# Kernel tuning notes

Hardware: AMD Instinct MI355X
Metric: run time of the kernel (lower is better)

## Reference

```python
import jax, jax.numpy as jnp
import numpy as np

N_LIG, N_TGT, E = 100000, 20000, 1000000
H = 128

def setup_inputs() -> dict:
    key = jax.random.key(0)
    ks = jax.random.split(key, 20)
    def lin(k, fan_in, fan_out):
        k1, k2 = jax.random.split(k)
        lim = 1.0 / np.sqrt(fan_in)
        W = jax.random.uniform(k1, (fan_in, fan_out), jnp.float32, -lim, lim)
        b = jax.random.uniform(k2, (fan_out,), jnp.float32, -lim, lim)
        return W, b
    W_lig, b_lig = lin(ks[0], 4, H)
    W_tgt, b_tgt = lin(ks[1], 1280, H)
    W1f, b1f = lin(ks[2], H, H)   # conv1 ligand->target
    W1r, b1r = lin(ks[3], H, H)   # conv1 target->ligand
    W2f, b2f = lin(ks[4], H, H)   # conv2 ligand->target
    W2r, b2r = lin(ks[5], H, H)   # conv2 target->ligand
    Wp1, bp1 = lin(ks[6], 2 * H, H)  # lin1
    Wp2, bp2 = lin(ks[7], H, 1)      # lin2
    return {
        'x_ligand': jax.random.normal(ks[8], (N_LIG, 4), jnp.float32),
        'x_target': jax.random.normal(ks[9], (N_TGT, 1280), jnp.float32),
        'edge_src': jax.random.randint(ks[10], (E,), 0, N_LIG, jnp.int32),
        'edge_dst': jax.random.randint(ks[11], (E,), 0, N_TGT, jnp.int32),
        'W_lig': W_lig, 'b_lig': b_lig, 'W_tgt': W_tgt, 'b_tgt': b_tgt,
        'W1f': W1f, 'b1f': b1f, 'W1r': W1r, 'b1r': b1r,
        'W2f': W2f, 'b2f': b2f, 'W2r': W2r, 'b2r': b2r,
        'Wp1': Wp1, 'bp1': bp1, 'Wp2': Wp2, 'bp2': bp2,
    }

def _mean_agg(feat, idx, num_segments):
    # scatter-mean: sum / count, 0 for isolated nodes (matches PyG 'mean')
    s = jax.ops.segment_sum(feat, idx, num_segments=num_segments)
    cnt = jax.ops.segment_sum(jnp.ones((idx.shape[0],), feat.dtype), idx,
                              num_segments=num_segments)
    return s / jnp.maximum(cnt, 1.0)[:, None]

def reference(x_ligand, x_target, edge_src, edge_dst,
              W_lig, b_lig, W_tgt, b_tgt,
              W1f, b1f, W1r, b1r, W2f, b2f, W2r, b2r,
              Wp1, bp1, Wp2, bp2):
    h_lig = x_ligand @ W_lig + b_lig   # [N_lig, H]
    h_tgt = x_target @ W_tgt + b_tgt   # [N_tgt, H]

    def conv(h_lig, h_tgt, Wf, bf, Wr, br):
        # ligand -> target (edges as given), target -> ligand (flipped edges)
        agg_t = _mean_agg(h_lig[edge_src], edge_dst, h_tgt.shape[0])
        agg_l = _mean_agg(h_tgt[edge_dst], edge_src, h_lig.shape[0])
        new_tgt = jax.nn.relu(agg_t @ Wf + bf)
        new_lig = jax.nn.relu(agg_l @ Wr + br)
        return new_lig, new_tgt

    h_lig, h_tgt = conv(h_lig, h_tgt, W1f, b1f, W1r, b1r)
    h_lig, h_tgt = conv(h_lig, h_tgt, W2f, b2f, W2r, b2r)

    # per-edge prediction (vectorized gather + tiny MLP), original loops edges
    combined = jnp.concatenate([h_lig[edge_src], h_tgt[edge_dst]], axis=-1)  # [E, 2H]
    pred = jax.nn.relu(combined @ Wp1 + bp1) @ Wp2 + bp2                     # [E, 1]
    return pred
```

## Files before the change

### kernel.cpp

```cpp
#include <hip/hip_runtime.h>
#include <hip/hip_bf16.h>

#define N_LIG 100000
#define N_TGT 20000
#define NEDGE 1000000
#define H 128
#define NXCD 8
#define RL 12500
#define RT 2500
#define CAP 131072
#define NSLICE 32

typedef __attribute__((ext_vector_type(8))) short short8v;
typedef __attribute__((ext_vector_type(4))) float f32x4;

__device__ __forceinline__ unsigned short f2bs(float f) {
    unsigned int u = __float_as_uint(f);
    u += 0x7fff + ((u >> 16) & 1);
    return (unsigned short)(u >> 16);
}
__device__ __forceinline__ float bs2f(unsigned int s) {
    return __uint_as_float(s << 16);
}

__global__ void transpose_w(const float* __restrict__ W, unsigned short* __restrict__ Wt, int K) {
    int idx = blockIdx.x * blockDim.x + threadIdx.x;
    if (idx >= K * 128) return;
    int k = idx >> 7, c = idx & 127;
    Wt[(size_t)c * K + k] = f2bs(W[idx]);
}

struct P6 { const float* w[6]; unsigned short* o[6]; };
__global__ void transpose6(P6 p) {
    int idx = blockIdx.x * blockDim.x + threadIdx.x;
    int which = idx >> 14;
    int rem = idx & 16383;
    int k = rem >> 7, c = rem & 127;
    p.o[which][(size_t)c * 128 + k] = f2bs(p.w[which][rem]);
}

__global__ void lin4_bf16(const float* __restrict__ X, const float* __restrict__ W,
                          const float* __restrict__ b, unsigned short* __restrict__ Y, int N) {
    int idx = blockIdx.x * blockDim.x + threadIdx.x;
    if (idx >= N * 16) return;
    int r = idx >> 4;
    int c = (idx & 15) * 8;
    float x0 = X[r * 4 + 0], x1 = X[r * 4 + 1], x2 = X[r * 4 + 2], x3 = X[r * 4 + 3];
    unsigned int o[4];
#pragma unroll
    for (int p = 0; p < 4; ++p) {
        float v0 = b[c + 2 * p] + x0 * W[c + 2 * p] + x1 * W[H + c + 2 * p] +
                   x2 * W[2 * H + c + 2 * p] + x3 * W[3 * H + c + 2 * p];
        float v1 = b[c + 2 * p + 1] + x0 * W[c + 2 * p + 1] + x1 * W[H + c + 2 * p + 1] +
                   x2 * W[2 * H + c + 2 * p + 1] + x3 * W[3 * H + c + 2 * p + 1];
        o[p] = (unsigned int)f2bs(v0) | ((unsigned int)f2bs(v1) << 16);
    }
    uint4 u = make_uint4(o[0], o[1], o[2], o[3]);
    *(uint4*)&Y[(size_t)r * H + c] = u;
}

__launch_bounds__(256)
__global__ void gemm_bf16(const unsigned short* __restrict__ X,
                          const float* __restrict__ Xf32,
                          const unsigned short* __restrict__ Wt,
                          const float* __restrict__ bias,
                          unsigned short* __restrict__ Y,
                          float* __restrict__ Yf,
                          int N, int K, int do_relu) {
    __shared__ unsigned short Ws[128 * 128];
    const int t = threadIdx.x;
    const int wv = t >> 6;
    const int lane = t & 63;
    const int lr = lane & 15;
    const int kb = lane >> 4;
    const int row0 = blockIdx.x * 64 + wv * 16;

    f32x4 acc[8];
#pragma unroll
    for (int i = 0; i < 8; ++i) acc[i] = (f32x4){0.f, 0.f, 0.f, 0.f};

    int arow = row0 + lr;
    if (arow >= N) arow = N - 1;
    const unsigned short* xrow = X ? X + (size_t)arow * K : nullptr;
    const float* xrowf = Xf32 ? Xf32 + (size_t)arow * K : nullptr;

    const int nch = K >> 7;
    for (int kc = 0; kc < nch; ++kc) {
        if (kc) __syncthreads();
#pragma unroll
        for (int i = 0; i < 8; ++i) {
            int li = t + i * 256;
            int r = li >> 4;
            int cb = (li & 15) << 4;
            int4 v = *(const int4*)(Wt + (size_t)r * K + (kc << 7) + (cb >> 1));
            *(int4*)((char*)Ws + r * 256 + (cb ^ ((r & 7) << 4))) = v;
        }
        short8v a[4];
        if (xrow) {
#pragma unroll
            for (int ks = 0; ks < 4; ++ks)
                a[ks] = *(const short8v*)(xrow + (kc << 7) + ks * 32 + kb * 8);
        } else {
#pragma unroll
            for (int ks = 0; ks < 4; ++ks) {
                const float* p = xrowf + (kc << 7) + ks * 32 + kb * 8;
                float4 f0 = *(const float4*)p;
                float4 f1 = *(const float4*)(p + 4);
                short8v av;
                av[0] = (short)f2bs(f0.x); av[1] = (short)f2bs(f0.y);
                av[2] = (short)f2bs(f0.z); av[3] = (short)f2bs(f0.w);
                av[4] = (short)f2bs(f1.x); av[5] = (short)f2bs(f1.y);
                av[6] = (short)f2bs(f1.z); av[7] = (short)f2bs(f1.w);
                a[ks] = av;
            }
        }
        __syncthreads();
#pragma unroll
        for (int ks = 0; ks < 4; ++ks) {
            int ofs = ks * 64 + kb * 16;
#pragma unroll
            for (int ct = 0; ct < 8; ++ct) {
                int c = ct * 16 + lr;
                short8v b = *(const short8v*)((const char*)Ws + c * 256 + (ofs ^ ((c & 7) << 4)));
                acc[ct] = __builtin_amdgcn_mfma_f32_16x16x32_bf16(a[ks], b, acc[ct], 0, 0, 0);
            }
        }
    }
#pragma unroll
    for (int ct = 0; ct < 8; ++ct) {
        int col = ct * 16 + lr;
        float bv = bias ? bias[col] : 0.f;
#pragma unroll
        for (int r = 0; r < 4; ++r) {
            int grow = row0 + kb * 4 + r;
            if (grow < N) {
                float v = acc[ct][r] + bv;
                if (do_relu) v = fmaxf(v, 0.f);
                if (Yf) Yf[(size_t)grow * H + col] = v;
                else    Y[(size_t)grow * H + col] = f2bs(v);
            }
        }
    }
}

__global__ void zero_gcur(int* __restrict__ g) {
    if (threadIdx.x < 16) g[threadIdx.x] = 0;
}

__launch_bounds__(256)
__global__ void bin_edges(const int* __restrict__ es, const int* __restrict__ ed,
                          unsigned long long* __restrict__ bkt_l, unsigned int* __restrict__ bkt_t,
                          int* __restrict__ gcur, int E) {
    __shared__ int h[16];
    __shared__ int base_s[16];
    int t = threadIdx.x;
    int lane = t & 63;
    if (t < 16) h[t] = 0;
    __syncthreads();
    int chunk = (E + gridDim.x - 1) / gridDim.x;
    int beg = blockIdx.x * chunk;
    int end = min(beg + chunk, E);
    for (int e0 = beg; e0 < end; e0 += 256) {
        int e = e0 + t;
        int bl = -1, bt = -1;
        if (e < end) { bl = es[e] / RL; bt = ed[e] / RT; }
#pragma unroll
        for (int b = 0; b < 8; ++b) {
            unsigned long long m = __ballot(bl == b);
            if (lane == 0 && m) atomicAdd(&h[b], __popcll(m));
            m = __ballot(bt == b);
            if (lane == 0 && m) atomicAdd(&h[8 + b], __popcll(m));
        }
    }
    __syncthreads();
    if (t < 16) {
        base_s[t] = atomicAdd(&gcur[t], h[t]);
        h[t] = 0;
    }
    __syncthreads();
    for (int e0 = beg; e0 < end; e0 += 256) {
        int e = e0 + t;
        int s = 0, d = 0, bl = -1, bt = -1;
        if (e < end) { s = es[e]; d = ed[e]; bl = s / RL; bt = d / RT; }
        unsigned int low = ((unsigned int)d << 17) | (unsigned int)s;
#pragma unroll
        for (int b = 0; b < 8; ++b) {
            unsigned long long m = __ballot(bl == b);
            if (m) {
                int leader = __ffsll((unsigned long long)m) - 1;
                int rank = __popcll(m & ((1ULL << lane) - 1ULL));
                int wbase = 0;
                if (lane == leader) wbase = atomicAdd(&h[b], __popcll(m));
                wbase = __shfl(wbase, leader);
                if (bl == b) {
                    int i = min(base_s[b] + wbase + rank, CAP - 1);
                    bkt_l[(size_t)b * CAP + i] = ((unsigned long long)(unsigned int)e << 32) | low;
                }
            }
            m = __ballot(bt == b);
            if (m) {
                int leader = __ffsll((unsigned long long)m) - 1;
                int rank = __popcll(m & ((1ULL << lane) - 1ULL));
                int wbase = 0;
                if (lane == leader) wbase = atomicAdd(&h[8 + b], __popcll(m));
                wbase = __shfl(wbase, leader);
                if (bt == b) {
                    int i = min(base_s[8 + b] + wbase + rank, CAP - 1);
                    bkt_t[(size_t)b * CAP + i] = low;
                }
            }
        }
    }
}

__launch_bounds__(256)
__global__ void count_slices(const unsigned long long* __restrict__ bkt_l,
                             const unsigned int* __restrict__ bkt_t,
                             const int* __restrict__ gcur,
                             int* __restrict__ cnts_l, int* __restrict__ cnts_t) {
    __shared__ int h[RL];
    int bi = blockIdx.x;
    int t = threadIdx.x;
    if (bi < 256) {
        int p = bi & 7, slice = bi >> 3;
        for (int j = t; j < RL; j += 256) h[j] = 0;
        __syncthreads();
        int n = min(gcur[p], CAP);
        int ss = (n + NSLICE - 1) / NSLICE;
        int beg = slice * ss, end = min(beg + ss, n);
        const unsigned long long* b = bkt_l + (size_t)p * CAP;
        for (int i = beg + t; i < end; i += 256)
            atomicAdd(&h[((unsigned int)b[i] & 0x1FFFF) - p * RL], 1);
        __syncthreads();
        int* dst = cnts_l + (size_t)slice * N_LIG + p * RL;
        for (int j = t; j < RL; j += 256) dst[j] = h[j];
    } else {
        int k = bi - 256;
        int p = k & 7, slice = k >> 3;
        for (int j = t; j < RT; j += 256) h[j] = 0;
        __syncthreads();
        int n = min(gcur[8 + p], CAP);
        int ss = (n + NSLICE - 1) / NSLICE;
        int beg = slice * ss, end = min(beg + ss, n);
        const unsigned int* b = bkt_t + (size_t)p * CAP;
        for (int i = beg + t; i < end; i += 256)
            atomicAdd(&h[(int)(b[i] >> 17) - p * RT], 1);
        __syncthreads();
        int* dst = cnts_t + (size_t)slice * N_TGT + p * RT;
        for (int j = t; j < RT; j += 256) dst[j] = h[j];
    }
}

__global__ void scan_block2(int* __restrict__ cnts_l, int* __restrict__ out_l,
                            int* __restrict__ bs_l, int nL, int nbL,
                            int* __restrict__ cnts_t, int* __restrict__ out_t,
                            int* __restrict__ bs_t, int nT) {
    __shared__ int ts[256];
    int* cnts; int* out; int* bsum; int n; int bi; size_t N;
    if ((int)blockIdx.x < nbL) { cnts = cnts_l; out = out_l; bsum = bs_l; n = nL; bi = blockIdx.x; N = N_LIG; }
    else { cnts = cnts_t; out = out_t; bsum = bs_t; n = nT; bi = blockIdx.x - nbL; N = N_TGT; }
    int t = threadIdx.x;
    int base = bi * 1024 + t * 4;
    int v[4] = {0, 0, 0, 0};
    for (int sl = 0; sl < NSLICE; ++sl) {
        size_t o = (size_t)sl * N + base;
#pragma unroll
        for (int i = 0; i < 4; i++) {
            if (base + i < n) {
                int c = cnts[o + i];
                cnts[o + i] = v[i];
                v[i] += c;
            }
        }
    }
    int s = v[0] + v[1] + v[2] + v[3];
    ts[t] = s;
    __syncthreads();
    for (int ofs = 1; ofs < 256; ofs <<= 1) {
        int x = (t >= ofs) ? ts[t - ofs] : 0;
        __syncthreads();
        ts[t] += x;
        __syncthreads();
    }
    int run = (t == 0) ? 0 : ts[t - 1];
    if (t == 255) bsum[bi] = ts[255];
#pragma unroll
    for (int i = 0; i < 4; i++) {
        if (base + i < n) out[base + i] = run;
        run += v[i];
    }
}

__global__ void scan_top2(int* __restrict__ bs_l, int nbL, int* __restrict__ bs_t, int nbT) {
    __shared__ int ts[256];
    int* bsum = (blockIdx.x == 0) ? bs_l : bs_t;
    int nb = (blockIdx.x == 0) ? nbL : nbT;
    int t = threadIdx.x;
    ts[t] = (t < nb) ? bsum[t] : 0;
    __syncthreads();
    for (int ofs = 1; ofs < 256; ofs <<= 1) {
        int x = (t >= ofs) ? ts[t - ofs] : 0;
        __syncthreads();
        ts[t] += x;
        __syncthreads();
    }
    int excl = (t == 0) ? 0 : ts[t - 1];
    if (t < nb) bsum[t] = excl;
}

__global__ void add_off2(int* __restrict__ rp_l, const int* __restrict__ bs_l,
                         int* __restrict__ rp_t, const int* __restrict__ bs_t) {
    int i = blockIdx.x * blockDim.x + threadIdx.x;
    if (i < N_LIG) {
        rp_l[i] += bs_l[i >> 10];
        if (i == 0) rp_l[N_LIG] = NEDGE;
    } else if (i < N_LIG + N_TGT) {
        int j = i - N_LIG;
        rp_t[j] += bs_t[j >> 10];
        if (j == 0) rp_t[N_TGT] = NEDGE;
    }
}

__launch_bounds__(256)
__global__ void fill_slices(const unsigned long long* __restrict__ bkt_l,
                            const unsigned int* __restrict__ bkt_t,
                            const int* __restrict__ gcur,
                            const int* __restrict__ rowptr_l, const int* __restrict__ rowptr_t,
                            const int* __restrict__ cnts_l, const int* __restrict__ cnts_t,
                            int2* __restrict__ elist_l, int* __restrict__ nbr_t) {
    __shared__ int cur[RL];
    int bi = blockIdx.x;
    int t = threadIdx.x;
    if (bi < 256) {
        int p = bi & 7, slice = bi >> 3;
        const int* rp = rowptr_l + p * RL;
        const int* pf = cnts_l + (size_t)slice * N_LIG + p * RL;
        for (int j = t; j < RL; j += 256) cur[j] = rp[j] + pf[j];
        __syncthreads();
        int n = min(gcur[p], CAP);
        int ss = (n + NSLICE - 1) / NSLICE;
        int beg = slice * ss, end = min(beg + ss, n);
        const unsigned long long* b = bkt_l + (size_t)p * CAP;
        for (int i = beg + t; i < end; i += 256) {
            unsigned long long v = b[i];
            unsigned int low = (unsigned int)v;
            int pos = atomicAdd(&cur[(low & 0x1FFFF) - p * RL], 1);
            elist_l[pos] = make_int2((low >> 17) & 0x7FFF, (int)(v >> 32));
        }
    } else {
        int k = bi - 256;
        int p = k & 7, slice = k >> 3;
        const int* rp = rowptr_t + p * RT;
        const int* pf = cnts_t + (size_t)slice * N_TGT + p * RT;
        for (int j = t; j < RT; j += 256) cur[j] = rp[j] + pf[j];
        __syncthreads();
        int n = min(gcur[8 + p], CAP);
        int ss = (n + NSLICE - 1) / NSLICE;
        int beg = slice * ss, end = min(beg + ss, n);
        const unsigned int* b = bkt_t + (size_t)p * CAP;
        for (int i = beg + t; i < end; i += 256) {
            unsigned int v = b[i];
            int pos = atomicAdd(&cur[(v >> 17) - p * RT], 1);
            nbr_t[pos] = v & 0x1FFFF;
        }
    }
}

__launch_bounds__(256)
__global__ void gather_mean_bf16(const unsigned short* __restrict__ feat,
                                 const int* __restrict__ rowptr, const int* __restrict__ nbr,
                                 int stride, const float* __restrict__ bias,
                                 unsigned short* __restrict__ out, int N) {
    int wid = (blockIdx.x * blockDim.x + threadIdx.x) >> 6;
    if (wid >= N) return;
    int lane = threadIdx.x & 63;
    int beg = rowptr[wid], end = rowptr[wid + 1];
    const unsigned int* f = (const unsigned int*)feat;
    float ax = 0.f, ay = 0.f;
    int j = beg;
    for (; j + 8 <= end; j += 8) {
        unsigned int v[8];
#pragma unroll
        for (int q = 0; q < 8; ++q) v[q] = f[(size_t)nbr[(j + q) * stride] * 64 + lane];
#pragma unroll
        for (int q = 0; q < 8; ++q) { ax += bs2f(v[q] & 0xffff); ay += bs2f(v[q] >> 16); }
    }
    for (; j + 2 <= end; j += 2) {
        unsigned int v0 = f[(size_t)nbr[(j + 0) * stride] * 64 + lane];
        unsigned int v1 = f[(size_t)nbr[(j + 1) * stride] * 64 + lane];
        ax += bs2f(v0 & 0xffff) + bs2f(v1 & 0xffff);
        ay += bs2f(v0 >> 16) + bs2f(v1 >> 16);
    }
    for (; j < end; ++j) {
        unsigned int v = f[(size_t)nbr[j * stride] * 64 + lane];
        ax += bs2f(v & 0xffff);
        ay += bs2f(v >> 16);
    }
    float inv = 1.f / (float)max(end - beg, 1);
    float mx = ax * inv, my = ay * inv;
    if (bias) {
        mx = fmaxf(mx + bias[2 * lane], 0.f);
        my = fmaxf(my + bias[2 * lane + 1], 0.f);
    }
    unsigned int o = (unsigned int)f2bs(mx) | ((unsigned int)f2bs(my) << 16);
    ((unsigned int*)out)[(size_t)wid * 64 + lane] = o;
}

__launch_bounds__(256)
__global__ void edge_mlp_csr(const unsigned short* __restrict__ A16, const unsigned short* __restrict__ B16,
                             const int* __restrict__ rowptr, const int2* __restrict__ elist,
                             const float* __restrict__ Wp2, const float* __restrict__ bp2,
                             float* __restrict__ out, int N) {
    int w = (blockIdx.x * blockDim.x + threadIdx.x) >> 6;
    if (w >= N) return;
    int lane = threadIdx.x & 63;
    int g = lane >> 4, l16 = lane & 15;
    int beg = rowptr[w], end = rowptr[w + 1];
    if (beg == end) return;
    uint4 ua = *(const uint4*)&A16[(size_t)w * H + l16 * 8];
    float a[8] = {bs2f(ua.x & 0xffff), bs2f(ua.x >> 16), bs2f(ua.y & 0xffff), bs2f(ua.y >> 16),
                  bs2f(ua.z & 0xffff), bs2f(ua.z >> 16), bs2f(ua.w & 0xffff), bs2f(ua.w >> 16)};
    float4 w0 = *(const float4*)&Wp2[l16 * 8];
    float4 w1 = *(const float4*)&Wp2[l16 * 8 + 4];
    float wv[8] = {w0.x, w0.y, w0.z, w0.w, w1.x, w1.y, w1.z, w1.w};
    float bp = bp2[0];
    for (int p = beg + g; p < end; p += 4) {
        int2 de = elist[p];
        uint4 ub = *(const uint4*)&B16[(size_t)de.x * H + l16 * 8];
        float bb[8] = {bs2f(ub.x & 0xffff), bs2f(ub.x >> 16), bs2f(ub.y & 0xffff), bs2f(ub.y >> 16),
                       bs2f(ub.z & 0xffff), bs2f(ub.z >> 16), bs2f(ub.w & 0xffff), bs2f(ub.w >> 16)};
        float acc = 0.f;
#pragma unroll
        for (int q = 0; q < 8; ++q) acc += fmaxf(a[q] + bb[q], 0.f) * wv[q];
        acc += __shfl_xor(acc, 8);
        acc += __shfl_xor(acc, 4);
        acc += __shfl_xor(acc, 2);
        acc += __shfl_xor(acc, 1);
        if (l16 == 0) out[de.y] = acc + bp;
    }
}

extern "C" void kernel_launch(void* const* d_in, const int* in_sizes, int n_in,
                              void* d_out, int out_size, void* d_ws, size_t ws_size,
                              hipStream_t stream) {
    const float* x_lig = (const float*)d_in[0];
    const float* x_tgt = (const float*)d_in[1];
    const int* es = (const int*)d_in[2];
    const int* ed = (const int*)d_in[3];
    const float* W_lig = (const float*)d_in[4];
    const float* b_lig = (const float*)d_in[5];
    const float* W_tgt = (const float*)d_in[6];
    const float* b_tgt = (const float*)d_in[7];
    const float* W1f = (const float*)d_in[8];
    const float* b1f = (const float*)d_in[9];
    const float* W1r = (const float*)d_in[10];
    const float* b1r = (const float*)d_in[11];
    const float* W2f = (const float*)d_in[12];
    const float* b2f = (const float*)d_in[13];
    const float* W2r = (const float*)d_in[14];
    const float* b2r = (const float*)d_in[15];
    const float* Wp1 = (const float*)d_in[16];
    const float* bp1 = (const float*)d_in[17];
    const float* Wp2 = (const float*)d_in[18];
    const float* bp2 = (const float*)d_in[19];
    float* out = (float*)d_out;

    char* base = (char*)d_ws;
    size_t off = 0;
    auto alloc = [&](size_t bytes) { char* p = base + off; off = (off + bytes + 255) & ~(size_t)255; return p; };
    unsigned short* L0 = (unsigned short*)alloc((size_t)N_LIG * H * 2);
    unsigned short* L1 = (unsigned short*)alloc((size_t)N_LIG * H * 2);
    unsigned short* T0 = (unsigned short*)alloc((size_t)N_TGT * H * 2);
    unsigned short* T1 = (unsigned short*)alloc((size_t)N_TGT * H * 2);
    unsigned short* G  = (unsigned short*)alloc((size_t)N_TGT * H * 2);
    unsigned short* Wt_tgt = (unsigned short*)alloc((size_t)128 * 1280 * 2);
    unsigned short* Wt1f = (unsigned short*)alloc(128 * 128 * 2);
    unsigned short* Wt1r = (unsigned short*)alloc(128 * 128 * 2);
    unsigned short* Wt2f = (unsigned short*)alloc(128 * 128 * 2);
    unsigned short* Wt2r = (unsigned short*)alloc(128 * 128 * 2);
    unsigned short* WtA = (unsigned short*)alloc(128 * 128 * 2);
    unsigned short* WtB = (unsigned short*)alloc(128 * 128 * 2);
    int* cnts_l = (int*)alloc((size_t)NSLICE * N_LIG * 4);
    int* cnts_t = (int*)alloc((size_t)NSLICE * N_TGT * 4);
    int* rowptr_l = (int*)alloc((N_LIG + 4) * 4);
    int* rowptr_t = (int*)alloc((N_TGT + 4) * 4);
    int* bsum_l = (int*)alloc(256 * 4);
    int* bsum_t = (int*)alloc(256 * 4);
    int* gcur = (int*)alloc(16 * 4);
    int2* elist_l = (int2*)alloc((size_t)NEDGE * 8);
    int* nbr_t = (int*)alloc((size_t)NEDGE * 4);
    unsigned long long* bkt_l = (unsigned long long*)alloc((size_t)NXCD * CAP * 8);
    unsigned int* bkt_t = (unsigned int*)alloc((size_t)NXCD * CAP * 4);

    const int ligBlocks = (N_LIG + 63) / 64;
    const int tgtBlocks = (N_TGT + 63) / 64;
    const int nbL = (N_LIG + 1023) / 1024;
    const int nbT = (N_TGT + 1023) / 1024;

    transpose_w<<<(1280 * 128 + 255) / 256, 256, 0, stream>>>(W_tgt, Wt_tgt, 1280);
    P6 p6;
    p6.w[0] = W1f; p6.o[0] = Wt1f;
    p6.w[1] = W1r; p6.o[1] = Wt1r;
    p6.w[2] = W2f; p6.o[2] = Wt2f;
    p6.w[3] = W2r; p6.o[3] = Wt2r;
    p6.w[4] = Wp1;           p6.o[4] = WtA;
    p6.w[5] = Wp1 + 128 * H; p6.o[5] = WtB;
    transpose6<<<6 * 64, 256, 0, stream>>>(p6);

    lin4_bf16<<<(N_LIG * 16 + 255) / 256, 256, 0, stream>>>(x_lig, W_lig, b_lig, L0, N_LIG);
    gemm_bf16<<<tgtBlocks, 256, 0, stream>>>(nullptr, x_tgt, Wt_tgt, b_tgt, T0, nullptr, N_TGT, 1280, 0);

    zero_gcur<<<1, 64, 0, stream>>>(gcur);
    bin_edges<<<512, 256, 0, stream>>>(es, ed, bkt_l, bkt_t, gcur, NEDGE);
    count_slices<<<512, 256, 0, stream>>>(bkt_l, bkt_t, gcur, cnts_l, cnts_t);
    scan_block2<<<nbL + nbT, 256, 0, stream>>>(cnts_l, rowptr_l, bsum_l, N_LIG, nbL,
                                               cnts_t, rowptr_t, bsum_t, N_TGT);
    scan_top2<<<2, 256, 0, stream>>>(bsum_l, nbL, bsum_t, nbT);
    add_off2<<<(N_LIG + N_TGT + 255) / 256, 256, 0, stream>>>(rowptr_l, bsum_l, rowptr_t, bsum_t);
    fill_slices<<<512, 256, 0, stream>>>(bkt_l, bkt_t, gcur, rowptr_l, rowptr_t,
                                         cnts_l, cnts_t, elist_l, nbr_t);

    const unsigned short* Wtf[2] = {Wt1f, Wt2f};
    const float* bfp[2] = {b1f, b2f};
    const unsigned short* Wtr[2] = {Wt1r, Wt2r};
    const float* brp[2] = {b1r, b2r};
    for (int layer = 0; layer < 2; ++layer) {
        gemm_bf16<<<tgtBlocks, 256, 0, stream>>>(T0, nullptr, Wtr[layer], nullptr, G, nullptr, N_TGT, 128, 0);
        gather_mean_bf16<<<(N_TGT * 64 + 255) / 256, 256, 0, stream>>>(L0, rowptr_t, nbr_t, 1, nullptr, T1, N_TGT);
        gather_mean_bf16<<<(N_LIG * 64 + 255) / 256, 256, 0, stream>>>(G, rowptr_l, (const int*)elist_l, 2, brp[layer], L0, N_LIG);
        gemm_bf16<<<tgtBlocks, 256, 0, stream>>>(T1, nullptr, Wtf[layer], bfp[layer], T0, nullptr, N_TGT, 128, 1);
    }

    gemm_bf16<<<ligBlocks, 256, 0, stream>>>(L0, nullptr, WtA, nullptr, L1, nullptr, N_LIG, 128, 0);
    gemm_bf16<<<tgtBlocks, 256, 0, stream>>>(T0, nullptr, WtB, bp1, T1, nullptr, N_TGT, 128, 0);

    edge_mlp_csr<<<(N_LIG * 64 + 255) / 256, 256, 0, stream>>>(
        L1, T1, rowptr_l, elist_l, Wp2, bp2, out, N_LIG);
}
```

Baseline: 459.7 us.

## Merge both mean-gathers into one launch with 16-byte loads across four edges

The two per-layer gather_mean kernels become a single gather2 launch. Its first N_TGT waves handle targets and the rest handle ligands. The ligand output now ping-pongs between two buffers, so the kernel no longer reads and writes L0 at the same time. Each wave now splits into four 16-lane groups that gather different edges with 128-bit loads per lane, then reduces the groups with cross-lane shuffles. This cuts the number of memory instructions and exposes more loads in flight. Non-temporal load and store hints are added to index reads and to the edge-MLP input and output, and the shuffle reduction adds some extra ALU work.

```diff
diff --git a/kernel.cpp b/kernel.cpp
--- a/kernel.cpp
+++ b/kernel.cpp
@@ -13,6 +13,7 @@
 
 typedef __attribute__((ext_vector_type(8))) short short8v;
 typedef __attribute__((ext_vector_type(4))) float f32x4;
+typedef __attribute__((ext_vector_type(4))) unsigned int uint4v;
 
 __device__ __forceinline__ unsigned short f2bs(float f) {
     unsigned int u = __float_as_uint(f);
@@ -367,43 +368,68 @@
 }
 
 __launch_bounds__(256)
-__global__ void gather_mean_bf16(const unsigned short* __restrict__ feat,
-                                 const int* __restrict__ rowptr, const int* __restrict__ nbr,
-                                 int stride, const float* __restrict__ bias,
-                                 unsigned short* __restrict__ out, int N) {
-    int wid = (blockIdx.x * blockDim.x + threadIdx.x) >> 6;
-    if (wid >= N) return;
+__global__ void gather2(const unsigned short* __restrict__ L_in, const int* __restrict__ rp_t,
+                        const int* __restrict__ nbr_t, unsigned short* __restrict__ T_out,
+                        const unsigned short* __restrict__ G, const int* __restrict__ rp_l,
+                        const int* __restrict__ elist2, const float* __restrict__ bias_r,
+                        unsigned short* __restrict__ L_out) {
+    int gwid = (blockIdx.x * blockDim.x + threadIdx.x) >> 6;
     int lane = threadIdx.x & 63;
-    int beg = rowptr[wid], end = rowptr[wid + 1];
-    const unsigned int* f = (const unsigned int*)feat;
-    float ax = 0.f, ay = 0.f;
-    int j = beg;
-    for (; j + 8 <= end; j += 8) {
-        unsigned int v[8];
-#pragma unroll
-        for (int q = 0; q < 8; ++q) v[q] = f[(size_t)nbr[(j + q) * stride] * 64 + lane];
-#pragma unroll
-        for (int q = 0; q < 8; ++q) { ax += bs2f(v[q] & 0xffff); ay += bs2f(v[q] >> 16); }
-    }
-    for (; j + 2 <= end; j += 2) {
-        unsigned int v0 = f[(size_t)nbr[(j + 0) * stride] * 64 + lane];
-        unsigned int v1 = f[(size_t)nbr[(j + 1) * stride] * 64 + lane];
-        ax += bs2f(v0 & 0xffff) + bs2f(v1 & 0xffff);
-        ay += bs2f(v0 >> 16) + bs2f(v1 >> 16);
-    }
-    for (; j < end; ++j) {
-        unsigned int v = f[(size_t)nbr[j * stride] * 64 + lane];
-        ax += bs2f(v & 0xffff);
-        ay += bs2f(v >> 16);
-    }
-    float inv = 1.f / (float)max(end - beg, 1);
-    float mx = ax * inv, my = ay * inv;
-    if (bias) {
-        mx = fmaxf(mx + bias[2 * lane], 0.f);
-        my = fmaxf(my + bias[2 * lane + 1], 0.f);
-    }
-    unsigned int o = (unsigned int)f2bs(mx) | ((unsigned int)f2bs(my) << 16);
-    ((unsigned int*)out)[(size_t)wid * 64 + lane] = o;
+    int g = lane >> 4, l16 = lane & 15;
+    const unsigned short* feat;
+    const int* rp;
+    const int* nbr;
+    int stride, wid;
+    const float* bias;
+    unsigned short* outp;
+    if (gwid < N_TGT) {
+        feat = L_in; rp = rp_t; nbr = nbr_t; stride = 1; bias = nullptr; outp = T_out; wid = gwid;
+    } else if (gwid < N_TGT + N_LIG) {
+        feat = G; rp = rp_l; nbr = elist2; stride = 2; bias = bias_r; outp = L_out; wid = gwid - N_TGT;
+    } else return;
+    int beg = rp[wid], end = rp[wid + 1];
+    const uint4v* f4 = (const uint4v*)feat;
+    float acc[8] = {0.f, 0.f, 0.f, 0.f, 0.f, 0.f, 0.f, 0.f};
+    int j = beg + g;
+    for (; j + 4 < end; j += 8) {
+        int n0 = __builtin_nontemporal_load(&nbr[j * stride]);
+        int n1 = __builtin_nontemporal_load(&nbr[(j + 4) * stride]);
+        uint4v v0 = f4[(size_t)n0 * 16 + l16];
+        uint4v v1 = f4[(size_t)n1 * 16 + l16];
+#pragma unroll
+        for (int q = 0; q < 4; ++q) {
+            acc[2 * q] += bs2f(v0[q] & 0xffff) + bs2f(v1[q] & 0xffff);
+            acc[2 * q + 1] += bs2f(v0[q] >> 16) + bs2f(v1[q] >> 16);
+        }
+    }
+    for (; j < end; j += 4) {
+        int n0 = __builtin_nontemporal_load(&nbr[j * stride]);
+        uint4v v0 = f4[(size_t)n0 * 16 + l16];
+#pragma unroll
+        for (int q = 0; q < 4; ++q) {
+            acc[2 * q] += bs2f(v0[q] & 0xffff);
+            acc[2 * q + 1] += bs2f(v0[q] >> 16);
+        }
+    }
+#pragma unroll
+    for (int q = 0; q < 8; ++q) {
+        acc[q] += __shfl_xor(acc[q], 16);
+        acc[q] += __shfl_xor(acc[q], 32);
+    }
+    if (g == 0) {
+        float inv = 1.f / (float)max(end - beg, 1);
+        uint4v o;
+#pragma unroll
+        for (int q = 0; q < 4; ++q) {
+            float m0 = acc[2 * q] * inv, m1 = acc[2 * q + 1] * inv;
+            if (bias) {
+                m0 = fmaxf(m0 + bias[l16 * 8 + 2 * q], 0.f);
+                m1 = fmaxf(m1 + bias[l16 * 8 + 2 * q + 1], 0.f);
+            }
+            o[q] = (unsigned int)f2bs(m0) | ((unsigned int)f2bs(m1) << 16);
+        }
+        ((uint4v*)outp)[(size_t)wid * 16 + l16] = o;
+    }
 }
 
 __launch_bounds__(256)
@@ -417,26 +443,29 @@
     int g = lane >> 4, l16 = lane & 15;
     int beg = rowptr[w], end = rowptr[w + 1];
     if (beg == end) return;
-    uint4 ua = *(const uint4*)&A16[(size_t)w * H + l16 * 8];
-    float a[8] = {bs2f(ua.x & 0xffff), bs2f(ua.x >> 16), bs2f(ua.y & 0xffff), bs2f(ua.y >> 16),
-                  bs2f(ua.z & 0xffff), bs2f(ua.z >> 16), bs2f(ua.w & 0xffff), bs2f(ua.w >> 16)};
+    uint4v ua = __builtin_nontemporal_load((const uint4v*)&A16[(size_t)w * H + l16 * 8]);
+    float a[8] = {bs2f(ua[0] & 0xffff), bs2f(ua[0] >> 16), bs2f(ua[1] & 0xffff), bs2f(ua[1] >> 16),
+                  bs2f(ua[2] & 0xffff), bs2f(ua[2] >> 16), bs2f(ua[3] & 0xffff), bs2f(ua[3] >> 16)};
     float4 w0 = *(const float4*)&Wp2[l16 * 8];
     float4 w1 = *(const float4*)&Wp2[l16 * 8 + 4];
     float wv[8] = {w0.x, w0.y, w0.z, w0.w, w1.x, w1.y, w1.z, w1.w};
     float bp = bp2[0];
     for (int p = beg + g; p < end; p += 4) {
-        int2 de = elist[p];
-        uint4 ub = *(const uint4*)&B16[(size_t)de.x * H + l16 * 8];
-        float bb[8] = {bs2f(ub.x & 0xffff), bs2f(ub.x >> 16), bs2f(ub.y & 0xffff), bs2f(ub.y >> 16),
-                       bs2f(ub.z & 0xffff), bs2f(ub.z >> 16), bs2f(ub.w & 0xffff), bs2f(ub.w >> 16)};
+        long long de2 = __builtin_nontemporal_load((const long long*)&elist[p]);
+        int d = (int)de2;
+        int e = (int)(de2 >> 32);
+        uint4v ub = *(const uint4v*)&B16[(size_t)d * H + l16 * 8];
         float acc = 0.f;
 #pragma unroll
-        for (int q = 0; q < 8; ++q) acc += fmaxf(a[q] + bb[q], 0.f) * wv[q];
+        for (int q = 0; q < 4; ++q) {
+            acc += fmaxf(a[2 * q] + bs2f(ub[q] & 0xffff), 0.f) * wv[2 * q];
+            acc += fmaxf(a[2 * q + 1] + bs2f(ub[q] >> 16), 0.f) * wv[2 * q + 1];
+        }
         acc += __shfl_xor(acc, 8);
         acc += __shfl_xor(acc, 4);
         acc += __shfl_xor(acc, 2);
         acc += __shfl_xor(acc, 1);
-        if (l16 == 0) out[de.y] = acc + bp;
+        if (l16 == 0) __builtin_nontemporal_store(acc + bp, &out[e]);
     }
 }
 
@@ -524,16 +553,20 @@
     const float* bfp[2] = {b1f, b2f};
     const unsigned short* Wtr[2] = {Wt1r, Wt2r};
     const float* brp[2] = {b1r, b2r};
+    unsigned short* Lcur = L0;
+    unsigned short* Lnxt = L1;
+    const int g2Blocks = (int)(((size_t)(N_TGT + N_LIG) * 64 + 255) / 256);
     for (int layer = 0; layer < 2; ++layer) {
         gemm_bf16<<<tgtBlocks, 256, 0, stream>>>(T0, nullptr, Wtr[layer], nullptr, G, nullptr, N_TGT, 128, 0);
-        gather_mean_bf16<<<(N_TGT * 64 + 255) / 256, 256, 0, stream>>>(L0, rowptr_t, nbr_t, 1, nullptr, T1, N_TGT);
-        gather_mean_bf16<<<(N_LIG * 64 + 255) / 256, 256, 0, stream>>>(G, rowptr_l, (const int*)elist_l, 2, brp[layer], L0, N_LIG);
+        gather2<<<g2Blocks, 256, 0, stream>>>(Lcur, rowptr_t, nbr_t, T1,
+                                              G, rowptr_l, (const int*)elist_l, brp[layer], Lnxt);
         gemm_bf16<<<tgtBlocks, 256, 0, stream>>>(T1, nullptr, Wtf[layer], bfp[layer], T0, nullptr, N_TGT, 128, 1);
+        unsigned short* tmp = Lcur; Lcur = Lnxt; Lnxt = tmp;
     }
 
     gemm_bf16<<<ligBlocks, 256, 0, stream>>>(L0, nullptr, WtA, nullptr, L1, nullptr, N_LIG, 128, 0);
     gemm_bf16<<<tgtBlocks, 256, 0, stream>>>(T0, nullptr, WtB, bp1, T1, nullptr, N_TGT, 128, 0);
 
-    edge_mlp_csr<<<(N_LIG * 64 + 255) / 256, 256, 0, stream>>>(
+    edge_mlp_csr<<<(int)(((size_t)N_LIG * 64 + 255) / 256), 256, 0, stream>>>(
         L1, T1, rowptr_l, elist_l, Wp2, bp2, out, N_LIG);
 }
```

Result: slower. 487.1 us (+6.0%).
